# Performance work log

Measured on AMD Instinct MI355X. Metric: run time of the kernel, lower is better.

The kernel has to match this reference:

```python
import jax, jax.numpy as jnp
import numpy as np
import math

D = 512
BT = 4096
N = 16
EPS = 1e-5

def layer_norm(x, g, b):
    mu = jnp.mean(x, axis=-1, keepdims=True)
    var = jnp.mean(jnp.square(x - mu), axis=-1, keepdims=True)
    return (x - mu) * jax.lax.rsqrt(var + EPS) * g + b

def setup_inputs() -> dict:
    key = jax.random.key(0)
    ks = jax.random.split(key, 8)
    x = jax.random.normal(ks[0], (BT, N, D), dtype=jnp.float32)
    # random bool mask (True = masked), but keep the diagonal unmasked so no
    # row is fully -inf (avoids NaN softmax, matching sane usage of the module)
    attn_mask = jax.random.randint(ks[1], (BT, N, N), 0, 2).astype(bool)
    eye = jnp.eye(N, dtype=bool)[None, :, :]
    attn_mask = jnp.where(eye, False, attn_mask)
    # LayerNorm params (torch init: weight=1, bias=0)
    g1 = jnp.ones((D,), jnp.float32); b1 = jnp.zeros((D,), jnp.float32)
    g2 = jnp.ones((D,), jnp.float32); b2 = jnp.zeros((D,), jnp.float32)
    # FFN params: Linear(D, 4D) then Linear(4D, D)
    s1 = 1.0 / math.sqrt(D)
    s2 = 1.0 / math.sqrt(4 * D)
    W1 = jax.random.uniform(ks[2], (D, 4 * D), jnp.float32, -s1, s1)
    bW1 = jax.random.uniform(ks[3], (4 * D,), jnp.float32, -s1, s1)
    W2 = jax.random.uniform(ks[4], (4 * D, D), jnp.float32, -s2, s2)
    bW2 = jax.random.uniform(ks[5], (D,), jnp.float32, -s2, s2)
    return {"x": x, "attn_mask": attn_mask, "g1": g1, "b1": b1,
            "g2": g2, "b2": b2, "W1": W1, "bW1": bW1, "W2": W2, "bW2": bW2}

def reference(x, attn_mask, g1, b1, g2, b2, W1, bW1, W2, bW2):
    d = x.shape[-1]
    # scores: [BT, N, N] = x x^T / sqrt(d)
    scores = jnp.einsum('bnd,bmd->bnm', x, x) / jnp.sqrt(jnp.asarray(d, x.dtype))
    scores = jnp.where(attn_mask, -jnp.inf, scores)
    attn = jax.nn.softmax(scores, axis=-1)
    out = jnp.einsum('bnm,bmd->bnd', attn, x)
    h = layer_norm(x + out, g1, b1)
    ff = jnp.maximum(h @ W1 + bW1, 0.0) @ W2 + bW2
    y = layer_norm(h + ff, g2, b2)
    return y, attn
```

## Files before the change

### kernel.cpp

```cpp
#include <hip/hip_runtime.h>

typedef float  f32x4 __attribute__((ext_vector_type(4)));
typedef short  short8 __attribute__((ext_vector_type(8)));

__device__ __forceinline__ unsigned short f2bf(float f) {
    unsigned u = __builtin_bit_cast(unsigned, f);
    unsigned r = u + 0x7FFFu + ((u >> 16) & 1u);
    return (unsigned short)(r >> 16);
}
__device__ __forceinline__ float bf2f(unsigned short b) {
    return __builtin_bit_cast(float, (unsigned)b << 16);
}

__device__ __forceinline__ f32x4 mfma16(short8 a, short8 b, f32x4 c) {
    return __builtin_amdgcn_mfma_f32_16x16x32_bf16(a, b, c, 0, 0, 0);
}

#define GLOAD16(gp, lp) \
    __builtin_amdgcn_global_load_lds((const __attribute__((address_space(1))) unsigned int*)(gp), \
                                     (__attribute__((address_space(3))) unsigned int*)(lp), 16, 0, 0)

#define BT   4096
#define NTOK 16
#define DDIM 512
#define Y_ELEMS 33554432ULL
#define XS_STRIDE 516

__global__ __launch_bounds__(256) void transpose_kernel(const float* __restrict__ in,
                                                        unsigned short* __restrict__ out,
                                                        int R, int C) {
    __shared__ float tile[32][33];
    const int tx = threadIdx.x & 31, ty = threadIdx.x >> 5;
    const int c0 = blockIdx.x * 32, r0 = blockIdx.y * 32;
#pragma unroll
    for (int i = 0; i < 4; ++i)
        tile[ty + 8 * i][tx] = in[(size_t)(r0 + ty + 8 * i) * C + c0 + tx];
    __syncthreads();
#pragma unroll
    for (int i = 0; i < 4; ++i)
        out[(size_t)(c0 + ty + 8 * i) * R + r0 + tx] = f2bf(tile[tx][ty + 8 * i]);
}

__global__ void detect_kernel(const unsigned char* __restrict__ m, int* __restrict__ flag) {
    __shared__ int any;
    if (threadIdx.x == 0) any = 0;
    __syncthreads();
    int loc = 0;
    for (int i = threadIdx.x; i < 4096; i += 256)
        if (i & 3) loc |= m[i];
    if (loc) atomicOr(&any, 1);
    __syncthreads();
    if (threadIdx.x == 0) *flag = any ? 1 : 0;
}

__global__ __launch_bounds__(256) void stage1_kernel(
    const float* __restrict__ x,
    const unsigned char* __restrict__ mask_u8, const int* __restrict__ mask_i32,
    const int* __restrict__ flagp,
    const float* __restrict__ g1, const float* __restrict__ b1,
    float* __restrict__ attn_out, unsigned short* __restrict__ hbf) {
    __shared__ float xs[NTOK * XS_STRIDE];
    __shared__ float p_lds[256];

    const int b = blockIdx.x, t = threadIdx.x;
    const float* xb = x + (size_t)b * (NTOK * DDIM);

#pragma unroll
    for (int i = 0; i < 8; ++i) {
        int s = t + 256 * i;
        int r = s >> 7, c4 = s & 127;
        f32x4 v = ((const f32x4*)xb)[s];
        *(f32x4*)(&xs[r * XS_STRIDE + c4 * 4]) = v;
    }
    __syncthreads();

    const int r = t >> 4, c = t & 15;
    {
        const f32x4* xr = (const f32x4*)(&xs[r * XS_STRIDE]);
        const f32x4* xc = (const f32x4*)(&xs[c * XS_STRIDE]);
        f32x4 d4 = {0.f, 0.f, 0.f, 0.f};
#pragma unroll 8
        for (int u = 0; u < 128; ++u) d4 += xr[u] * xc[u];
        float s_rc = (d4.x + d4.y + d4.z + d4.w) * 0.04419417382415922f;

        const int flag = *flagp;
        size_t midx = (size_t)b * 256 + t;
        bool msk = flag ? (mask_u8[midx] != 0) : (mask_i32[midx] != 0);
        float sv = msk ? -1e30f : s_rc;
        float mx = sv;
        mx = fmaxf(mx, __shfl_xor(mx, 1, 16));
        mx = fmaxf(mx, __shfl_xor(mx, 2, 16));
        mx = fmaxf(mx, __shfl_xor(mx, 4, 16));
        mx = fmaxf(mx, __shfl_xor(mx, 8, 16));
        float e = msk ? 0.f : expf(sv - mx);
        float sum = e;
        sum += __shfl_xor(sum, 1, 16);
        sum += __shfl_xor(sum, 2, 16);
        sum += __shfl_xor(sum, 4, 16);
        sum += __shfl_xor(sum, 8, 16);
        float p = e / sum;
        p_lds[t] = p;
        attn_out[midx] = p;
    }
    __syncthreads();

    const int r2 = t >> 4, tc = t & 15;
    f32x4 acc[8];
#pragma unroll
    for (int j = 0; j < 8; ++j) acc[j] = (f32x4){0.f, 0.f, 0.f, 0.f};
    for (int c2 = 0; c2 < 16; ++c2) {
        float pw = p_lds[r2 * 16 + c2];
        const f32x4* xrow = (const f32x4*)(&xs[c2 * XS_STRIDE]);
#pragma unroll
        for (int j = 0; j < 8; ++j) acc[j] += pw * xrow[tc + 16 * j];
    }

    const f32x4* xme = (const f32x4*)(&xs[r2 * XS_STRIDE]);
    f32x4 vv[8];
    float s1 = 0.f, s2 = 0.f;
#pragma unroll
    for (int j = 0; j < 8; ++j) {
        f32x4 v = xme[tc + 16 * j] + acc[j];
        vv[j] = v;
        s1 += v.x + v.y + v.z + v.w;
        s2 += v.x * v.x + v.y * v.y + v.z * v.z + v.w * v.w;
    }
    s1 += __shfl_xor(s1, 1, 16); s2 += __shfl_xor(s2, 1, 16);
    s1 += __shfl_xor(s1, 2, 16); s2 += __shfl_xor(s2, 2, 16);
    s1 += __shfl_xor(s1, 4, 16); s2 += __shfl_xor(s2, 4, 16);
    s1 += __shfl_xor(s1, 8, 16); s2 += __shfl_xor(s2, 8, 16);
    float mu = s1 * (1.f / 512.f);
    float var = s2 * (1.f / 512.f) - mu * mu;
    float inv = rsqrtf(var + 1e-5f);

    unsigned short* hrow = hbf + (size_t)(b * NTOK + r2) * DDIM;
#pragma unroll
    for (int j = 0; j < 8; ++j) {
        int u = tc + 16 * j;
        f32x4 gv = ((const f32x4*)g1)[u];
        f32x4 bv = ((const f32x4*)b1)[u];
        f32x4 o = (vv[j] - mu) * inv * gv + bv;
        uint2 pk;
        pk.x = (unsigned)f2bf(o.x) | ((unsigned)f2bf(o.y) << 16);
        pk.y = (unsigned)f2bf(o.z) | ((unsigned)f2bf(o.w) << 16);
        *(uint2*)(hrow + u * 4) = pk;
    }
}

#define PH_READA(Al, Q) { short8 a00, a01, a10, a11; \
    a00 = *(const short8*)((Al) + aoffs[2*(Q)]   + kk2[0]); \
    a01 = *(const short8*)((Al) + aoffs[2*(Q)]   + kk2[1]); \
    a10 = *(const short8*)((Al) + aoffs[2*(Q)+1] + kk2[0]); \
    a11 = *(const short8*)((Al) + aoffs[2*(Q)+1] + kk2[1]);

#define PH_READB(Bl) \
    bb00 = *(const short8*)((Bl) + boffs[0] + kk2[0]); \
    bb01 = *(const short8*)((Bl) + boffs[0] + kk2[1]); \
    bb10 = *(const short8*)((Bl) + boffs[1] + kk2[0]); \
    bb11 = *(const short8*)((Bl) + boffs[1] + kk2[1]); \
    bb20 = *(const short8*)((Bl) + boffs[2] + kk2[0]); \
    bb21 = *(const short8*)((Bl) + boffs[2] + kk2[1]); \
    bb30 = *(const short8*)((Bl) + boffs[3] + kk2[0]); \
    bb31 = *(const short8*)((Bl) + boffs[3] + kk2[1]);

#define PH_MFMA(Q) \
    asm volatile("s_waitcnt lgkmcnt(0)" ::: "memory"); \
    __builtin_amdgcn_sched_barrier(0); \
    __builtin_amdgcn_s_setprio(1); \
    acc[2*(Q)][0]   = mfma16(a00, bb00, acc[2*(Q)][0]); \
    acc[2*(Q)][0]   = mfma16(a01, bb01, acc[2*(Q)][0]); \
    acc[2*(Q)][1]   = mfma16(a00, bb10, acc[2*(Q)][1]); \
    acc[2*(Q)][1]   = mfma16(a01, bb11, acc[2*(Q)][1]); \
    acc[2*(Q)][2]   = mfma16(a00, bb20, acc[2*(Q)][2]); \
    acc[2*(Q)][2]   = mfma16(a01, bb21, acc[2*(Q)][2]); \
    acc[2*(Q)][3]   = mfma16(a00, bb30, acc[2*(Q)][3]); \
    acc[2*(Q)][3]   = mfma16(a01, bb31, acc[2*(Q)][3]); \
    acc[2*(Q)+1][0] = mfma16(a10, bb00, acc[2*(Q)+1][0]); \
    acc[2*(Q)+1][0] = mfma16(a11, bb01, acc[2*(Q)+1][0]); \
    acc[2*(Q)+1][1] = mfma16(a10, bb10, acc[2*(Q)+1][1]); \
    acc[2*(Q)+1][1] = mfma16(a11, bb11, acc[2*(Q)+1][1]); \
    acc[2*(Q)+1][2] = mfma16(a10, bb20, acc[2*(Q)+1][2]); \
    acc[2*(Q)+1][2] = mfma16(a11, bb21, acc[2*(Q)+1][2]); \
    acc[2*(Q)+1][3] = mfma16(a10, bb30, acc[2*(Q)+1][3]); \
    acc[2*(Q)+1][3] = mfma16(a11, bb31, acc[2*(Q)+1][3]); \
    __builtin_amdgcn_s_setprio(0);

#define PH_END  __builtin_amdgcn_s_barrier(); }

#define GEMM_BODY(MORE) \
        PH_READA(A0lds, 0) PH_READB(B0lds) \
        stageA(v, A1lds, 0); stageA(v, A1lds, 1); \
        PH_MFMA(0) PH_END \
        PH_READA(A0lds, 1) \
        if (MORE) stageB(u2, B0lds, 0); \
        PH_MFMA(1) PH_END \
        PH_READA(A0lds, 2) \
        if (MORE) stageB(u2, B0lds, 1); \
        PH_MFMA(2) PH_END \
        PH_READA(A0lds, 3) \
        PH_MFMA(3) \
        if (MORE) { asm volatile("s_waitcnt vmcnt(4)" ::: "memory"); } \
        else      { asm volatile("s_waitcnt vmcnt(0)" ::: "memory"); } \
        PH_END \
        PH_READA(A1lds, 0) PH_READB(B1lds) \
        if (MORE) stageA(u2, A0lds, 0); \
        PH_MFMA(0) PH_END \
        PH_READA(A1lds, 1) \
        if (MORE) stageA(u2, A0lds, 1); \
        PH_MFMA(1) PH_END \
        PH_READA(A1lds, 2) \
        if (MORE) stageB(v2, B1lds, 0); \
        PH_MFMA(2) PH_END \
        PH_READA(A1lds, 3) \
        if (MORE) stageB(v2, B1lds, 1); \
        PH_MFMA(3) \
        if (MORE) { asm volatile("s_waitcnt vmcnt(4)" ::: "memory"); } \
        PH_END

__global__ __launch_bounds__(512, 2) void gemm1_kernel(
    const unsigned short* __restrict__ A, const unsigned short* __restrict__ Bw,
    const float* __restrict__ bias, unsigned short* __restrict__ Cbf) {
    constexpr int K = 512;
    constexpr int NT = K / 64;
    constexpr int NXT = 8;
    constexpr int NC = 2048;

    extern __shared__ unsigned short lds[];
    unsigned short* A0lds = lds;
    unsigned short* B0lds = lds + 16384;
    unsigned short* A1lds = lds + 32768;
    unsigned short* B1lds = lds + 49152;

    const int nwg = (int)gridDim.x;
    const int orig = (int)blockIdx.x;
    const int q8 = nwg >> 3, r8 = nwg & 7;
    const int xcd = orig & 7, idx = orig >> 3;
    const int w = (xcd < r8 ? xcd * (q8 + 1) : r8 * (q8 + 1) + (xcd - r8) * q8) + idx;
    const int mt_i = w / NXT, nt_i = w % NXT;
    const size_t arow0 = (size_t)mt_i * 256;
    const int n0 = nt_i * 256;

    const int tid = threadIdx.x;
    const int l = tid & 63, wv = tid >> 6;
    const int wm = wv >> 2, wn = wv & 3;
    const int lr = l & 15, lq = l >> 4;

    const int srow = tid >> 3;
    const int skb = ((((tid & 7) << 4) ^ ((srow & 7) << 4)) >> 1);

    const int sw = (lr & 7) << 4;
    int kk2[2];
    kk2[0] = ((lq * 16) ^ sw) >> 1;
    kk2[1] = ((64 + lq * 16) ^ sw) >> 1;
    int aoffs[8], boffs[4];
#pragma unroll
    for (int mf = 0; mf < 8; ++mf) aoffs[mf] = (wm * 128 + mf * 16 + lr) * 64;
#pragma unroll
    for (int nf = 0; nf < 4; ++nf) boffs[nf] = (wn * 64 + nf * 16 + lr) * 64;

    f32x4 acc[8][4];
#pragma unroll
    for (int i = 0; i < 8; ++i)
#pragma unroll
        for (int j = 0; j < 4; ++j) acc[i][j] = (f32x4){0.f, 0.f, 0.f, 0.f};

    short8 bb00, bb01, bb10, bb11, bb20, bb21, bb30, bb31;

    const unsigned short* Ath = A + (arow0 + srow) * (size_t)K + skb;
    const unsigned short* Bth = Bw + ((size_t)n0 + srow) * K + skb;

    auto stageA = [&](int tile, unsigned short* dst, int half) {
        const unsigned short* g = Ath + (size_t)half * (128 * K) + tile * 64;
        unsigned short* d = dst + half * 8192 + tid * 8;
        GLOAD16(g, d);
        GLOAD16(g + (size_t)64 * K, d + 4096);
    };
    auto stageB = [&](int tile, unsigned short* dst, int half) {
        const unsigned short* g = Bth + (size_t)half * (128 * K) + tile * 64;
        unsigned short* d = dst + half * 8192 + tid * 8;
        GLOAD16(g, d);
        GLOAD16(g + (size_t)64 * K, d + 4096);
    };

    stageB(0, B0lds, 0);
    stageB(0, B0lds, 1);
    stageA(0, A0lds, 0);
    stageA(0, A0lds, 1);
    stageB(1, B1lds, 0);
    stageB(1, B1lds, 1);
    asm volatile("s_waitcnt vmcnt(4)" ::: "memory");
    __builtin_amdgcn_s_barrier();

#pragma unroll 1
    for (int t = 0; t < NT / 2 - 1; ++t) {
        const int v = 2 * t + 1, u2 = 2 * t + 2, v2 = 2 * t + 3;
        GEMM_BODY(1)
    }
    {
        const int t = NT / 2 - 1;
        const int v = 2 * t + 1, u2 = 2 * t + 2, v2 = 2 * t + 3;
        (void)u2; (void)v2;
        GEMM_BODY(0)
    }

    float bv[4];
#pragma unroll
    for (int nf = 0; nf < 4; ++nf) bv[nf] = bias[n0 + wn * 64 + nf * 16 + lr];

#pragma unroll
    for (int mf = 0; mf < 8; ++mf) {
#pragma unroll
        for (int qq = 0; qq < 4; ++qq) {
            long row = (long)arow0 + wm * 128 + mf * 16 + lq * 4 + qq;
#pragma unroll
            for (int nf = 0; nf < 4; ++nf) {
                int col = n0 + wn * 64 + nf * 16 + lr;
                float vvv = acc[mf][nf][qq] + bv[nf];
                Cbf[(size_t)row * NC + col] = f2bf(fmaxf(vvv, 0.f));
            }
        }
    }
}


#define RD_A2(Al) \
    areg[0][0] = *(const short8*)((Al) + aoffs2[0] + kk2[0]); \
    areg[0][1] = *(const short8*)((Al) + aoffs2[0] + kk2[1]); \
    areg[1][0] = *(const short8*)((Al) + aoffs2[1] + kk2[0]); \
    areg[1][1] = *(const short8*)((Al) + aoffs2[1] + kk2[1]); \
    areg[2][0] = *(const short8*)((Al) + aoffs2[2] + kk2[0]); \
    areg[2][1] = *(const short8*)((Al) + aoffs2[2] + kk2[1]); \
    areg[3][0] = *(const short8*)((Al) + aoffs2[3] + kk2[0]); \
    areg[3][1] = *(const short8*)((Al) + aoffs2[3] + kk2[1]);

#define RD_B2(Bl, q) \
    bq00 = *(const short8*)((Bl) + boffs2[2*(q)]   + kk2[0]); \
    bq01 = *(const short8*)((Bl) + boffs2[2*(q)]   + kk2[1]); \
    bq10 = *(const short8*)((Bl) + boffs2[2*(q)+1] + kk2[0]); \
    bq11 = *(const short8*)((Bl) + boffs2[2*(q)+1] + kk2[1]);

#define MM_Q2(q) \
    asm volatile("s_waitcnt lgkmcnt(0)" ::: "memory"); \
    __builtin_amdgcn_sched_barrier(0); \
    __builtin_amdgcn_s_setprio(1); \
    _Pragma("unroll") \
    for (int mf = 0; mf < 4; ++mf) { \
        acc[mf][2*(q)]   = mfma16(areg[mf][0], bq00, acc[mf][2*(q)]); \
        acc[mf][2*(q)]   = mfma16(areg[mf][1], bq01, acc[mf][2*(q)]); \
        acc[mf][2*(q)+1] = mfma16(areg[mf][0], bq10, acc[mf][2*(q)+1]); \
        acc[mf][2*(q)+1] = mfma16(areg[mf][1], bq11, acc[mf][2*(q)+1]); \
    } \
    __builtin_amdgcn_s_setprio(0);

#define BAR2 __builtin_amdgcn_s_barrier();

#define BODY2(MORE) \
         \
        RD_A2(A0l) RD_B2(B0l, 0) \
        stageB(v, B1l, 0); \
        MM_Q2(0) BAR2 \
         \
        RD_B2(B0l, 1) \
        stageB(v, B1l, 1); \
        if (MORE) stageA(u2, A0l); \
        MM_Q2(1) BAR2 \
         \
        RD_B2(B0l, 2) \
        MM_Q2(2) BAR2 \
         \
        RD_B2(B0l, 3) \
        MM_Q2(3) \
        if (MORE) { asm volatile("s_waitcnt vmcnt(2)" ::: "memory"); } \
        else      { asm volatile("s_waitcnt vmcnt(0)" ::: "memory"); } \
        BAR2 \
         \
        RD_A2(A1l) RD_B2(B1l, 0) \
        if (MORE) stageB(u2, B0l, 0); \
        MM_Q2(0) BAR2 \
         \
        RD_B2(B1l, 1) \
        if (MORE) { stageB(u2, B0l, 1); stageA(v2, A1l); } \
        MM_Q2(1) BAR2 \
         \
        RD_B2(B1l, 2) \
        MM_Q2(2) BAR2 \
         \
        RD_B2(B1l, 3) \
        MM_Q2(3) \
        if (MORE) { asm volatile("s_waitcnt vmcnt(2)" ::: "memory"); } \
        else      { asm volatile("s_waitcnt vmcnt(0)" ::: "memory"); } \
        BAR2

__global__ __launch_bounds__(512, 2) void gemm2ln_kernel(
    const unsigned short* __restrict__ A,
    const unsigned short* __restrict__ Bw,
    const float* __restrict__ bias,
    const unsigned short* __restrict__ hres,
    const float* __restrict__ g2, const float* __restrict__ b2,
    float* __restrict__ y, long out_row0) {
    constexpr int K = 2048;
    constexpr int NT = K / 64;

    extern __shared__ unsigned short lds[];
    unsigned short* A0l = lds;
    unsigned short* A1l = lds + 8192;
    unsigned short* B0l = lds + 16384;
    unsigned short* B1l = lds + 49152;

    const int nwg = (int)gridDim.x;
    const int orig = (int)blockIdx.x;
    const int q8 = nwg >> 3, r8 = nwg & 7;
    const int xcd = orig & 7, idx = orig >> 3;
    const int w = (xcd < r8 ? xcd * (q8 + 1) : r8 * (q8 + 1) + (xcd - r8) * q8) + idx;
    const size_t arow0 = (size_t)w * 128;

    const int tid = threadIdx.x;
    const int l = tid & 63, wv = tid >> 6;
    const int wm = wv & 1, wn = wv >> 1;
    const int lr = l & 15, lq = l >> 4;

    const int srow = tid >> 3;
    const int skb = ((((tid & 7) << 4) ^ ((srow & 7) << 4)) >> 1);

    const int sw = (lr & 7) << 4;
    int kk2[2];
    kk2[0] = ((lq * 16) ^ sw) >> 1;
    kk2[1] = ((64 + lq * 16) ^ sw) >> 1;
    int aoffs2[4], boffs2[8];
#pragma unroll
    for (int mf = 0; mf < 4; ++mf) aoffs2[mf] = (wm * 64 + mf * 16 + lr) * 64;
#pragma unroll
    for (int nf = 0; nf < 8; ++nf) boffs2[nf] = (wn * 128 + nf * 16 + lr) * 64;

    f32x4 acc[4][8];
#pragma unroll
    for (int i = 0; i < 4; ++i)
#pragma unroll
        for (int j = 0; j < 8; ++j) acc[i][j] = (f32x4){0.f, 0.f, 0.f, 0.f};

    short8 areg[4][2];
    short8 bq00, bq01, bq10, bq11;

    const unsigned short* Ath = A + (arow0 + srow) * (size_t)K + skb;
    const unsigned short* Bth = Bw + (size_t)srow * K + skb;

    auto stageA = [&](int tile, unsigned short* dst) {
        const unsigned short* g = Ath + tile * 64;
        unsigned short* d = dst + tid * 8;
        GLOAD16(g, d);
        GLOAD16(g + (size_t)64 * K, d + 4096);
    };
    auto stageB = [&](int tile, unsigned short* dst, int half) {
        const unsigned short* g = Bth + (size_t)(half * 256) * K + tile * 64;
        unsigned short* d = dst + half * 16384 + tid * 8;
#pragma unroll
        for (int i = 0; i < 4; ++i)
            GLOAD16(g + (size_t)(64 * i) * K, d + 4096 * i);
    };

    stageA(0, A0l);
    stageB(0, B0l, 0);
    stageB(0, B0l, 1);
    stageA(1, A1l);
    asm volatile("s_waitcnt vmcnt(2)" ::: "memory");
    __builtin_amdgcn_s_barrier();

#pragma unroll 1
    for (int t = 0; t < NT / 2 - 1; ++t) {
        const int v = 2 * t + 1, u2 = 2 * t + 2, v2 = 2 * t + 3;
        BODY2(1)
    }
    {
        const int t = NT / 2 - 1;
        const int v = 2 * t + 1, u2 = 2 * t + 2, v2 = 2 * t + 3;
        (void)u2; (void)v2;
        BODY2(0)
    }

    float* red = (float*)lds;
    float bv2[8], gv2[8], bb2[8];
#pragma unroll
    for (int nf = 0; nf < 8; ++nf) {
        int col = wn * 128 + nf * 16 + lr;
        bv2[nf] = bias[col];
        gv2[nf] = g2[col];
        bb2[nf] = b2[col];
    }

#pragma unroll
    for (int mf = 0; mf < 4; ++mf) {
#pragma unroll
        for (int qq = 0; qq < 4; ++qq) {
            int lrow = wm * 64 + mf * 16 + lq * 4 + qq;
            long grow = out_row0 + (long)arow0 + lrow;
            const unsigned short* hr = hres + (size_t)grow * 512 + wn * 128 + lr;
            float s = 0.f, s2 = 0.f;
#pragma unroll
            for (int nf = 0; nf < 8; ++nf) {
                float z = acc[mf][nf][qq] + bv2[nf] + bf2f(hr[nf * 16]);
                acc[mf][nf][qq] = z;
                s += z;
                s2 += z * z;
            }
            s += __shfl_xor(s, 1, 16); s2 += __shfl_xor(s2, 1, 16);
            s += __shfl_xor(s, 2, 16); s2 += __shfl_xor(s2, 2, 16);
            s += __shfl_xor(s, 4, 16); s2 += __shfl_xor(s2, 4, 16);
            s += __shfl_xor(s, 8, 16); s2 += __shfl_xor(s2, 8, 16);
            if (lr == 0) {
                red[wn * 128 + lrow] = s;
                red[512 + wn * 128 + lrow] = s2;
            }
        }
    }
    __syncthreads();

#pragma unroll
    for (int mf = 0; mf < 4; ++mf) {
#pragma unroll
        for (int qq = 0; qq < 4; ++qq) {
            int lrow = wm * 64 + mf * 16 + lq * 4 + qq;
            long grow = out_row0 + (long)arow0 + lrow;
            float s = red[lrow] + red[128 + lrow] + red[256 + lrow] + red[384 + lrow];
            float s2 = red[512 + lrow] + red[640 + lrow] + red[768 + lrow] + red[896 + lrow];
            float mu = s * (1.f / 512.f);
            float var = s2 * (1.f / 512.f) - mu * mu;
            float inv = rsqrtf(var + 1e-5f);
            float* yr = y + (size_t)grow * 512 + wn * 128 + lr;
#pragma unroll
            for (int nf = 0; nf < 8; ++nf)
                yr[nf * 16] = (acc[mf][nf][qq] - mu) * inv * gv2[nf] + bb2[nf];
        }
    }
}

extern "C" void kernel_launch(void* const* d_in, const int* in_sizes, int n_in,
                              void* d_out, int out_size, void* d_ws, size_t ws_size,
                              hipStream_t stream) {
    const float* x = (const float*)d_in[0];
    const void* mask = d_in[1];
    const float* g1 = (const float*)d_in[2];
    const float* b1 = (const float*)d_in[3];
    const float* g2 = (const float*)d_in[4];
    const float* b2 = (const float*)d_in[5];
    const float* W1 = (const float*)d_in[6];
    const float* bW1 = (const float*)d_in[7];
    const float* W2 = (const float*)d_in[8];
    const float* bW2 = (const float*)d_in[9];

    float* y = (float*)d_out;
    float* attn = y + Y_ELEMS;
    char* ws = (char*)d_ws;
    unsigned short* W1T = (unsigned short*)(ws);
    unsigned short* W2T = (unsigned short*)(ws + 2097152);
    int* flag = (int*)(ws + 4194304);
    unsigned short* h = (unsigned short*)(ws + 4194560);
    unsigned short* t1 = (unsigned short*)(ws + 71303424ULL);

    hipFuncSetAttribute((const void*)gemm1_kernel,
                        hipFuncAttributeMaxDynamicSharedMemorySize, 131072);
    hipFuncSetAttribute((const void*)gemm2ln_kernel,
                        hipFuncAttributeMaxDynamicSharedMemorySize, 163840);

    long cap256 = ((long)ws_size - 71303424L) / (256L * 2048L * 2L);
    if (cap256 < 1) cap256 = 1;
    if (cap256 > 256) cap256 = 256;

    transpose_kernel<<<dim3(64, 16), dim3(256), 0, stream>>>(W1, W1T, 512, 2048);
    transpose_kernel<<<dim3(16, 64), dim3(256), 0, stream>>>(W2, W2T, 2048, 512);
    detect_kernel<<<1, 256, 0, stream>>>((const unsigned char*)mask, flag);
    stage1_kernel<<<4096, 256, 0, stream>>>(x, (const unsigned char*)mask, (const int*)mask,
                                            flag, g1, b1, attn, h);
    for (long t0 = 0; t0 < 256; t0 += cap256) {
        long mt = (256 - t0 < cap256) ? (256 - t0) : cap256;
        long row0 = t0 * 256;
        gemm1_kernel<<<dim3((unsigned)(8 * mt)), 512, 131072, stream>>>(
            h + (size_t)row0 * 512, W1T, bW1, t1);
        gemm2ln_kernel<<<dim3((unsigned)(2 * mt)), 512, 163840, stream>>>(
            t1, W2T, bW2, h, g2, b2, y, row0);
    }
}
```

Measured before the change: 404.2 us.

## Permute GEMM2 K dimension to pack GEMM1 epilogue stores as 8-byte writes

W2's transposed copy is permuted along K so that each lane's four ReLU outputs from GEMM1 can sit contiguously in the t1 intermediate. This replaces four scattered 2-byte stores per row with one packed 8-byte store. The permutation is consistent because GEMM2 reduces over K, so the same reordering applied to both t1 columns and W2T rows keeps the result unchanged. The GEMM2 loop also issues B-fragment LDS reads before A-fragment reads. The correctness risk is that the permutation must exactly match the epilogue's column mapping.

```diff
diff --git a/kernel.cpp b/kernel.cpp
--- a/kernel.cpp
+++ b/kernel.cpp
@@ -28,7 +28,7 @@
 
 __global__ __launch_bounds__(256) void transpose_kernel(const float* __restrict__ in,
                                                         unsigned short* __restrict__ out,
-                                                        int R, int C) {
+                                                        int R, int C, int perm) {
     __shared__ float tile[32][33];
     const int tx = threadIdx.x & 31, ty = threadIdx.x >> 5;
     const int c0 = blockIdx.x * 32, r0 = blockIdx.y * 32;
@@ -36,9 +36,11 @@
     for (int i = 0; i < 4; ++i)
         tile[ty + 8 * i][tx] = in[(size_t)(r0 + ty + 8 * i) * C + c0 + tx];
     __syncthreads();
+    const int k = r0 + tx;
+    const int kp = perm ? ((k & ~63) | ((k & 15) << 2) | ((k >> 4) & 3)) : k;
 #pragma unroll
     for (int i = 0; i < 4; ++i)
-        out[(size_t)(c0 + ty + 8 * i) * R + r0 + tx] = f2bf(tile[tx][ty + 8 * i]);
+        out[(size_t)(c0 + ty + 8 * i) * R + kp] = f2bf(tile[tx][ty + 8 * i]);
 }
 
 __global__ void detect_kernel(const unsigned char* __restrict__ m, int* __restrict__ flag) {
@@ -312,12 +314,14 @@
 #pragma unroll
         for (int qq = 0; qq < 4; ++qq) {
             long row = (long)arow0 + wm * 128 + mf * 16 + lq * 4 + qq;
-#pragma unroll
-            for (int nf = 0; nf < 4; ++nf) {
-                int col = n0 + wn * 64 + nf * 16 + lr;
-                float vvv = acc[mf][nf][qq] + bv[nf];
-                Cbf[(size_t)row * NC + col] = f2bf(fmaxf(vvv, 0.f));
-            }
+            unsigned short o0 = f2bf(fmaxf(acc[mf][0][qq] + bv[0], 0.f));
+            unsigned short o1 = f2bf(fmaxf(acc[mf][1][qq] + bv[1], 0.f));
+            unsigned short o2 = f2bf(fmaxf(acc[mf][2][qq] + bv[2], 0.f));
+            unsigned short o3 = f2bf(fmaxf(acc[mf][3][qq] + bv[3], 0.f));
+            uint2 pk;
+            pk.x = (unsigned)o0 | ((unsigned)o1 << 16);
+            pk.y = (unsigned)o2 | ((unsigned)o3 << 16);
+            *(uint2*)(&Cbf[(size_t)row * NC + n0 + wn * 64 + lr * 4]) = pk;
         }
     }
 }
@@ -355,36 +359,30 @@
 #define BAR2 __builtin_amdgcn_s_barrier();
 
 #define BODY2(MORE) \
-         \
-        RD_A2(A0l) RD_B2(B0l, 0) \
+        RD_B2(B0l, 0) \
+        RD_A2(A0l) \
         stageB(v, B1l, 0); \
         MM_Q2(0) BAR2 \
-         \
         RD_B2(B0l, 1) \
         stageB(v, B1l, 1); \
         if (MORE) stageA(u2, A0l); \
         MM_Q2(1) BAR2 \
-         \
         RD_B2(B0l, 2) \
         MM_Q2(2) BAR2 \
-         \
         RD_B2(B0l, 3) \
         MM_Q2(3) \
         if (MORE) { asm volatile("s_waitcnt vmcnt(2)" ::: "memory"); } \
         else      { asm volatile("s_waitcnt vmcnt(0)" ::: "memory"); } \
         BAR2 \
-         \
-        RD_A2(A1l) RD_B2(B1l, 0) \
+        RD_B2(B1l, 0) \
+        RD_A2(A1l) \
         if (MORE) stageB(u2, B0l, 0); \
         MM_Q2(0) BAR2 \
-         \
         RD_B2(B1l, 1) \
         if (MORE) { stageB(u2, B0l, 1); stageA(v2, A1l); } \
         MM_Q2(1) BAR2 \
-         \
         RD_B2(B1l, 2) \
         MM_Q2(2) BAR2 \
-         \
         RD_B2(B1l, 3) \
         MM_Q2(3) \
         if (MORE) { asm volatile("s_waitcnt vmcnt(2)" ::: "memory"); } \
@@ -565,8 +563,8 @@
     if (cap256 < 1) cap256 = 1;
     if (cap256 > 256) cap256 = 256;
 
-    transpose_kernel<<<dim3(64, 16), dim3(256), 0, stream>>>(W1, W1T, 512, 2048);
-    transpose_kernel<<<dim3(16, 64), dim3(256), 0, stream>>>(W2, W2T, 2048, 512);
+    transpose_kernel<<<dim3(64, 16), dim3(256), 0, stream>>>(W1, W1T, 512, 2048, 0);
+    transpose_kernel<<<dim3(16, 64), dim3(256), 0, stream>>>(W2, W2T, 2048, 512, 1);
     detect_kernel<<<1, 256, 0, stream>>>((const unsigned char*)mask, flag);
     stage1_kernel<<<4096, 256, 0, stream>>>(x, (const unsigned char*)mask, (const int*)mask,
                                             flag, g1, b1, attn, h);
```

New measurement: 393.4 us. 2.7% less time.
